# Kernel optimization log

Hardware: AMD Instinct MI355X
Metric: run time of the kernel (lower is better)

The kernel has to match this reference:

```python
import jax, jax.numpy as jnp
import numpy as np

IN_C, OUT_C, K, UP, C_DIM = 128, 64, 3, 2, 512
CLAMP = 256.0
ACT_GAIN = np.sqrt(2.0)  # lrelu def_gain


def _upfirdn_up2(x, f2):
    """upfirdn2d with up=2, padding=(3,2,3,2), gain=up^2 for a 4-tap filter.

    Padding values come from conv2d_resample: p = k//2 = 1, fw = 4, up = 2 =>
    px0 = p + (fw+up-1)//2 = 3, px1 = p + (fw-up)//2 = 2.
    """
    N, C, H, W = x.shape
    px0, px1 = 3, 2
    # zero-insert upsample (interior padding) fused with edge padding;
    # trailing zero of the up-sampled signal folded into the high pad.
    x = jax.lax.pad(x, jnp.asarray(0, x.dtype),
                    ((0, 0, 0), (0, 0, 0),
                     (px0, px1 + (UP - 1), UP - 1),
                     (px0, px1 + (UP - 1), UP - 1)))
    k = (f2 * (UP * UP)).astype(x.dtype)[None, None]   # [1,1,4,4], symmetric -> flip is a no-op
    k = jnp.tile(k, (C, 1, 1, 1))                       # depthwise FIR
    return jax.lax.conv_general_dilated(
        x, k, window_strides=(1, 1), padding='VALID',
        feature_group_count=C, dimension_numbers=('NCHW', 'OIHW', 'NCHW'))


def setup_inputs() -> dict:
    key = jax.random.key(0)
    ks = jax.random.split(key, 4)
    return {
        "x": jax.random.normal(ks[0], (8, IN_C, 128, 128), jnp.float32),
        "c": jax.random.normal(ks[1], (8, C_DIM), jnp.float32),
        "weight": jax.random.normal(ks[2], (OUT_C, IN_C, K, K), jnp.float32),
        "bias": jnp.zeros((OUT_C,), jnp.float32),
        "w_affine": jax.random.normal(ks[3], (IN_C, C_DIM), jnp.float32),
        "b_affine": jnp.zeros((IN_C,), jnp.float32),
    }


def reference(x, c, weight, bias, w_affine, b_affine):
    # setup_filter: normalize separable FIR taps
    f1 = jnp.array([1.0, 3.0, 3.0, 1.0], jnp.float32)
    f1 = f1 / jnp.sum(f1)
    f2 = jnp.outer(f1, f1)

    # hyper modulation: x *= 1 + tanh(affine(c))
    y = c @ (w_affine * (1.0 / np.sqrt(C_DIM))).T + b_affine   # FullyConnectedLayer, linear
    x = x * (1.0 + jnp.tanh(y))[:, :, None, None]

    # conv2d_resample(up=2, padding=k//2, flip_weight=False)
    w = weight * (1.0 / np.sqrt(IN_C * K * K))                  # weight_gain
    x = _upfirdn_up2(x, f2)                                      # [N,C,2H+2,2W+2]
    w = w[:, :, ::-1, ::-1]                                      # flip_weight=False => true convolution
    x = jax.lax.conv_general_dilated(
        x, w.astype(x.dtype), window_strides=(1, 1), padding='VALID',
        dimension_numbers=('NCHW', 'OIHW', 'NCHW'))              # [N,OUT_C,2H,2W]

    # bias_act: lrelu(x+b)*sqrt(2), clamp at +-256 (gain=1)
    x = jax.nn.leaky_relu(x + bias[None, :, None, None], 0.2) * ACT_GAIN
    return jnp.clip(x, -CLAMP, CLAMP)
```

## Files before the change

kernel.cpp:

```cpp
#include <hip/hip_runtime.h>
#include <math.h>

#define IN_C   128
#define OUT_C  64
#define CDIM   512
#define HW     128
#define PHW    130
#define OHW    256
#define NB     8

typedef __attribute__((ext_vector_type(8))) short short8;
typedef __attribute__((ext_vector_type(4))) float f32x4;

__device__ inline unsigned short f2bf(float f) {
    unsigned int u = __float_as_uint(f);
    unsigned int r = (u + 0x7fffu + ((u >> 16) & 1u)) >> 16;
    return (unsigned short)r;
}

__device__ inline float postact(float v) {
    v = v > 0.f ? v : 0.2f * v;
    v *= 1.4142135623730951f;
    return fminf(fmaxf(v, -256.f), 256.f);
}

__device__ __forceinline__ void gload16(const void* g, void* l) {
    __builtin_amdgcn_global_load_lds(
        (const __attribute__((address_space(1))) unsigned int*)g,
        (__attribute__((address_space(3))) unsigned int*)l, 16, 0, 0);
}

__global__ __launch_bounds__(256) void prep_kernel(
    const float* __restrict__ w, unsigned short* __restrict__ wb2,
    unsigned short* __restrict__ xg,
    const float* __restrict__ c, const float* __restrict__ wa,
    const float* __restrict__ ba, float* __restrict__ gain) {
    int blk = blockIdx.x;
    if (blk < 1152) {
        int idx  = blk * 256 + threadIdx.x;
        int e    = idx & 7;
        int lane = (idx >> 3) & 63;
        int pr   = (idx >> 9) & 31;
        int kt   = idx >> 14;
        int hh = pr >> 4, kcb = (pr >> 3) & 1, wM = (pr >> 2) & 1, fi = pr & 3;
        int m   = (wM * 8 + hh * 4 + fi) * 16 + (lane & 15);
        int ic  = (kt & 1) * 64 + kcb * 32 + (lane >> 4) * 8 + e;
        int tap = kt >> 1;
        int ky = tap / 3, kx = tap % 3;
        int oc = m >> 2, ph = m & 3;
        int py = ph >> 1, px = ph & 1;
        int sy = 2 * ky + (py == 0 ? 1 : 0);
        int sx = 2 * kx + (px == 0 ? 1 : 0);
        const float k1[4] = {0.25f, 0.75f, 0.75f, 0.25f};
        float sum = 0.f;
        #pragma unroll
        for (int by = 0; by < 3; ++by) {
            int ay = sy - by;
            if (ay < 0 || ay > 3) continue;
            #pragma unroll
            for (int bx = 0; bx < 3; ++bx) {
                int ax = sx - bx;
                if (ax < 0 || ax > 3) continue;
                sum += w[((oc * IN_C + ic) * 3 + (2 - by)) * 3 + (2 - bx)] * k1[ay] * k1[ax];
            }
        }
        wb2[idx] = f2bf(sum * 0.029462782549439483f);
    } else if (blk < 1410) {
        int id = (blk - 1152) * 256 + threadIdx.x;
        int cc = id & 15;
        int t  = id >> 4;
        int p  = t % 516;
        int n  = t / 516;
        int Y, X;
        if (p < 130)      { Y = 0;   X = p; }
        else if (p < 260) { Y = 129; X = p - 130; }
        else              { int q = p - 260; Y = 1 + (q >> 1); X = (q & 1) * 129; }
        uint4 z = make_uint4(0, 0, 0, 0);
        *reinterpret_cast<uint4*>(xg + (((size_t)(n * PHW) + Y) * PHW + X) * 128 + cc * 8) = z;
    } else {
        int wave = (blk - 1410) * 4 + (threadIdx.x >> 6);
        int lane = threadIdx.x & 63;
        int n  = wave >> 7;
        int ic = wave & 127;
        const float* cp = c + n * CDIM;
        const float* wp = wa + ic * CDIM;
        float s = 0.f;
        #pragma unroll
        for (int k = 0; k < CDIM / 64; ++k) s += cp[lane + 64 * k] * wp[lane + 64 * k];
        #pragma unroll
        for (int off = 32; off > 0; off >>= 1) s += __shfl_down(s, off);
        if (lane == 0) {
            float y = s * 0.04419417382415922f + ba[ic];
            gain[n * IN_C + ic] = 1.0f + tanhf(y);
        }
    }
}

__global__ __launch_bounds__(256) void xprep_kernel(const float* __restrict__ x,
                                                    const float* __restrict__ gain,
                                                    unsigned short* __restrict__ xg) {
    int n = blockIdx.x >> 7;
    int y = blockIdx.x & 127;
    __shared__ unsigned short lds[128][130];
    int tid = threadIdx.x;
    for (int i = tid; i < 128 * 128; i += 256) {
        int ic = i >> 7, pix = i & 127;
        float v = x[(((n * IN_C + ic) * HW) + y) * HW + pix] * gain[n * IN_C + ic];
        lds[pix][ic] = f2bf(v);
    }
    __syncthreads();
    unsigned int* dst = (unsigned int*)(xg + (((size_t)(n * PHW) + y + 1) * PHW + 1) * 128);
    for (int i = tid; i < 8192; i += 256) {
        int pix = i >> 6, d = i & 63;
        int j = d >> 2, ww = d & 3;
        int js = j ^ ((pix + 1) & 7);
        dst[pix * 64 + js * 4 + ww] = *reinterpret_cast<const unsigned int*>(&lds[pix][d * 2]);
    }
}

#define BARRIER() do { __builtin_amdgcn_sched_barrier(0); __builtin_amdgcn_s_barrier(); __builtin_amdgcn_sched_barrier(0); } while (0)
#define MM(ACC, AF, BF) ACC = __builtin_amdgcn_mfma_f32_16x16x32_bf16(AF, BF, ACC, 0, 0, 0)

__global__ __launch_bounds__(512, 2) void conv_mfma4(
    const unsigned short* __restrict__ xg,
    const unsigned short* __restrict__ wb2,
    const float* __restrict__ bias,
    float* __restrict__ out) {
    __shared__ __align__(16) char smem[148480];

    const int bid = blockIdx.x;
    const int wg  = ((bid & 7) << 6) + (bid >> 3);
    const int n     = wg >> 6;
    const int patch = wg & 63;
    const int Y0 = (patch >> 3) * 16;
    const int X0 = (patch & 7) * 16;
    const int tid  = threadIdx.x;
    const int lane = tid & 63;
    const int wid  = tid >> 6;
    const int wM = wid >> 2;
    const int wN = wid & 3;
    const int l16 = lane & 15;
    const int lhi = lane >> 4;
    const int pbase = wN * 4;

    const char* xgb = (const char*)xg + (size_t)n * PHW * PHW * 256;
    const char* wbb = (const char*)wb2;
    char* haloB = smem + 65536;

    #pragma unroll 1
    for (int i = 0; i < 11; ++i) {
        int cc = i * 512 + tid;
        if (cc < 5184) {
            int r = cc / 288;
            int t2 = cc - r * 288;
            gload16(xgb + ((size_t)(Y0 + r) * PHW + X0) * 256 + t2 * 16,
                    haloB + (i * 512 + wid * 64) * 16);
        }
    }

    auto stageA = [&](int k, int hh, int half) {
        gload16(wbb + k * 32768 + hh * 16384 + half * 8192 + tid * 16,
                smem + ((k & 1) << 15) + hh * 16384 + half * 8192 + wid * 1024);
    };

    f32x4 acc[8][4];
    #pragma unroll
    for (int f = 0; f < 8; ++f)
        #pragma unroll
        for (int b = 0; b < 4; ++b) acc[f][b] = (f32x4)0.f;

    stageA(0, 0, 0); stageA(0, 0, 1);
    stageA(0, 1, 0); stageA(0, 1, 1);
    stageA(1, 0, 0); stageA(1, 0, 1);
    asm volatile("s_waitcnt vmcnt(4)" ::: "memory");
    BARRIER();

    #pragma unroll 1
    for (int t = 0; t < 18; ++t) {
        const char* bA = smem + ((t & 1) << 15);
        const int tap = t >> 1;
        const int h   = t & 1;
        const int ky  = tap / 3;
        const int kx  = tap - ky * 3;
        const int C   = l16 + kx;
        const int bswz = (C & 7) << 4;

        auto ldB1 = [&](int b, int kc) -> short8 {
            int icoff = ((h << 7) + (kc << 6) + (lhi << 4)) ^ bswz;
            return *reinterpret_cast<const short8*>(
                haloB + ((pbase + b + ky) * 18 + C) * 256 + icoff);
        };

        short8 Af[8], Bf0[4], Bf1[4];

        #pragma unroll
        for (int f = 0; f < 4; ++f)
            #pragma unroll
            for (int kc = 0; kc < 2; ++kc)
                Af[f * 2 + kc] = *reinterpret_cast<const short8*>(
                    bA + ((kc * 8 + wM * 4 + f) << 10) + (lane << 4));
        #pragma unroll
        for (int b = 0; b < 2; ++b)
            #pragma unroll
            for (int kc = 0; kc < 2; ++kc) Bf0[b * 2 + kc] = ldB1(b, kc);
        if (t + 1 < 18) stageA(t + 1, 1, 0);
        BARRIER();
        __builtin_amdgcn_s_setprio(1);
        #pragma unroll
        for (int f = 0; f < 4; ++f)
            #pragma unroll
            for (int b = 0; b < 2; ++b) {
                MM(acc[f][b], Af[f * 2 + 0], Bf0[b * 2 + 0]);
                MM(acc[f][b], Af[f * 2 + 1], Bf0[b * 2 + 1]);
            }
        __builtin_amdgcn_s_setprio(0);

        #pragma unroll
        for (int b = 0; b < 2; ++b)
            #pragma unroll
            for (int kc = 0; kc < 2; ++kc) Bf1[b * 2 + kc] = ldB1(b + 2, kc);
        if (t + 1 < 18) stageA(t + 1, 1, 1);
        if (t < 17) { asm volatile("s_waitcnt vmcnt(4)" ::: "memory"); }
        else        { asm volatile("s_waitcnt vmcnt(0)" ::: "memory"); }
        BARRIER();
        __builtin_amdgcn_s_setprio(1);
        #pragma unroll
        for (int f = 0; f < 4; ++f)
            #pragma unroll
            for (int b = 0; b < 2; ++b) {
                MM(acc[f][b + 2], Af[f * 2 + 0], Bf1[b * 2 + 0]);
                MM(acc[f][b + 2], Af[f * 2 + 1], Bf1[b * 2 + 1]);
            }
        __builtin_amdgcn_s_setprio(0);

        #pragma unroll
        for (int f = 0; f < 4; ++f)
            #pragma unroll
            for (int kc = 0; kc < 2; ++kc)
                Af[f * 2 + kc] = *reinterpret_cast<const short8*>(
                    bA + ((16 + kc * 8 + wM * 4 + f) << 10) + (lane << 4));
        if (t + 2 < 18) stageA(t + 2, 0, 0);
        BARRIER();
        __builtin_amdgcn_s_setprio(1);
        #pragma unroll
        for (int f = 0; f < 4; ++f)
            #pragma unroll
            for (int b = 0; b < 2; ++b) {
                MM(acc[4 + f][b], Af[f * 2 + 0], Bf0[b * 2 + 0]);
                MM(acc[4 + f][b], Af[f * 2 + 1], Bf0[b * 2 + 1]);
            }
        __builtin_amdgcn_s_setprio(0);

        if (t + 2 < 18) stageA(t + 2, 0, 1);
        if (t < 16)       { asm volatile("s_waitcnt vmcnt(4)" ::: "memory"); }
        else if (t == 16) { asm volatile("s_waitcnt vmcnt(2)" ::: "memory"); }
        BARRIER();
        __builtin_amdgcn_s_setprio(1);
        #pragma unroll
        for (int f = 0; f < 4; ++f)
            #pragma unroll
            for (int b = 0; b < 2; ++b) {
                MM(acc[4 + f][b + 2], Af[f * 2 + 0], Bf1[b * 2 + 0]);
                MM(acc[4 + f][b + 2], Af[f * 2 + 1], Bf1[b * 2 + 1]);
            }
        __builtin_amdgcn_s_setprio(0);
    }

    #pragma unroll
    for (int f = 0; f < 8; ++f) {
        const int oc = wM * 32 + f * 4 + lhi;
        const float bi = bias[oc];
        #pragma unroll
        for (int b = 0; b < 4; ++b) {
            const int ypix = Y0 + pbase + b;
            const int xpix = X0 + l16;
            float* o0 = out + (((size_t)(n * OUT_C + oc) * OHW) + 2 * ypix) * OHW + 2 * xpix;
            float2 v0 = make_float2(postact(acc[f][b][0] + bi), postact(acc[f][b][1] + bi));
            float2 v1 = make_float2(postact(acc[f][b][2] + bi), postact(acc[f][b][3] + bi));
            *reinterpret_cast<float2*>(o0) = v0;
            *reinterpret_cast<float2*>(o0 + OHW) = v1;
        }
    }
}

__global__ void gain_kernel(const float* __restrict__ c,
                            const float* __restrict__ w_affine,
                            const float* __restrict__ b_affine,
                            float* __restrict__ gain) {
    int wave = (blockIdx.x * blockDim.x + threadIdx.x) >> 6;
    int lane = threadIdx.x & 63;
    if (wave >= NB * IN_C) return;
    int n  = wave >> 7;
    int ic = wave & 127;
    const float* cp = c + n * CDIM;
    const float* wp = w_affine + ic * CDIM;
    float s = 0.f;
    #pragma unroll
    for (int k = 0; k < CDIM / 64; ++k) s += cp[lane + 64 * k] * wp[lane + 64 * k];
    #pragma unroll
    for (int off = 32; off > 0; off >>= 1) s += __shfl_down(s, off);
    if (lane == 0) {
        float y = s * 0.04419417382415922f + b_affine[ic];
        gain[n * IN_C + ic] = 1.0f + tanhf(y);
    }
}

__global__ void wprep_kernel(const float* __restrict__ w, float* __restrict__ wp) {
    int idx = blockIdx.x * blockDim.x + threadIdx.x;
    if (idx >= IN_C * 9 * 4 * OUT_C) return;
    int oc = idx & 63;
    int t  = idx >> 6;
    int ph = t & 3;  t >>= 2;
    int kx = t % 3;  t /= 3;
    int ky = t % 3;  t /= 3;
    int ic = t;
    int py = ph >> 1, px = ph & 1;
    int sy = 2 * ky + (py == 0 ? 1 : 0);
    int sx = 2 * kx + (px == 0 ? 1 : 0);
    const float k1[4] = {0.25f, 0.75f, 0.75f, 0.25f};
    float sum = 0.f;
    #pragma unroll
    for (int by = 0; by < 3; ++by) {
        int ay = sy - by;
        if (ay < 0 || ay > 3) continue;
        #pragma unroll
        for (int bx = 0; bx < 3; ++bx) {
            int ax = sx - bx;
            if (ax < 0 || ax > 3) continue;
            sum += w[((oc * IN_C + ic) * 3 + (2 - by)) * 3 + (2 - bx)] * k1[ay] * k1[ax];
        }
    }
    wp[idx] = sum * 0.029462782549439483f;
}

__global__ __launch_bounds__(256) void conv_main(
    const float* __restrict__ x, const float* __restrict__ gain,
    const float* __restrict__ wp, const float* __restrict__ bias,
    float* __restrict__ out) {
    const int n    = blockIdx.z >> 3;
    const int occ  = (blockIdx.z & 7) * 8;
    const int tx0  = blockIdx.x * 16;
    const int ty0  = blockIdx.y * 16;
    const int tid  = threadIdx.x;
    const int lx   = tid & 15;
    const int ly   = tid >> 4;
    __shared__ float xsf[8][18][18];
    float acc[4][8];
    #pragma unroll
    for (int p = 0; p < 4; ++p)
        #pragma unroll
        for (int o = 0; o < 8; ++o) acc[p][o] = 0.f;
    for (int ic0 = 0; ic0 < IN_C; ic0 += 8) {
        __syncthreads();
        for (int i = tid; i < 8 * 324; i += 256) {
            int icb = i / 324;
            int rem = i - icb * 324;
            int yy  = rem / 18;
            int xx  = rem - yy * 18;
            int gy  = ty0 + yy - 1;
            int gx  = tx0 + xx - 1;
            int ic  = ic0 + icb;
            float v = 0.f;
            if (gy >= 0 && gy < HW && gx >= 0 && gx < HW)
                v = x[((n * IN_C + ic) * HW + gy) * HW + gx] * gain[n * IN_C + ic];
            xsf[icb][yy][xx] = v;
        }
        __syncthreads();
        for (int icb = 0; icb < 8; ++icb) {
            const int ic = ic0 + icb;
            const float* wpp = wp + ic * (9 * 4 * OUT_C) + occ;
            #pragma unroll
            for (int ky = 0; ky < 3; ++ky)
                #pragma unroll
                for (int kx = 0; kx < 3; ++kx) {
                    float tv = xsf[icb][ly + ky][lx + kx];
                    const float* w9 = wpp + (ky * 3 + kx) * (4 * OUT_C);
                    #pragma unroll
                    for (int p = 0; p < 4; ++p)
                        #pragma unroll
                        for (int o = 0; o < 8; ++o)
                            acc[p][o] = fmaf(tv, w9[p * OUT_C + o], acc[p][o]);
                }
        }
    }
    const int ybase = 2 * (ty0 + ly);
    const int xbase = 2 * (tx0 + lx);
    #pragma unroll
    for (int o = 0; o < 8; ++o) {
        float b = bias[occ + o];
        #pragma unroll
        for (int py = 0; py < 2; ++py) {
            float2 v;
            v.x = postact(acc[py * 2 + 0][o] + b);
            v.y = postact(acc[py * 2 + 1][o] + b);
            *reinterpret_cast<float2*>(
                &out[((size_t)(n * OUT_C + occ + o) * OHW + (ybase + py)) * OHW + xbase]) = v;
        }
    }
}

extern "C" void kernel_launch(void* const* d_in, const int* in_sizes, int n_in,
                              void* d_out, int out_size, void* d_ws, size_t ws_size,
                              hipStream_t stream) {
    const float* x        = (const float*)d_in[0];
    const float* c        = (const float*)d_in[1];
    const float* weight   = (const float*)d_in[2];
    const float* bias     = (const float*)d_in[3];
    const float* w_affine = (const float*)d_in[4];
    const float* b_affine = (const float*)d_in[5];
    float* out = (float*)d_out;

    float* gain = (float*)d_ws;

    const size_t NEED = 1048576 + (size_t)NB * PHW * PHW * IN_C * 2;
    if (ws_size >= NEED) {
        unsigned short* wb2 = (unsigned short*)((char*)d_ws + 8192);
        unsigned short* xg  = (unsigned short*)((char*)d_ws + 1048576);
        prep_kernel<<<dim3(1666), dim3(256), 0, stream>>>(weight, wb2, xg, c, w_affine, b_affine, gain);
        xprep_kernel<<<dim3(NB * HW), dim3(256), 0, stream>>>(x, gain, xg);
        conv_mfma4<<<dim3(512), dim3(512), 0, stream>>>(xg, wb2, bias, out);
    } else {
        float* wp = (float*)((char*)d_ws + 8192);
        gain_kernel<<<dim3((NB * IN_C * 64) / 256), dim3(256), 0, stream>>>(c, w_affine, b_affine, gain);
        wprep_kernel<<<dim3((IN_C * 9 * 4 * OUT_C + 255) / 256), dim3(256), 0, stream>>>(weight, wp);
        conv_main<<<dim3(HW / 16, HW / 16, NB * 8), dim3(256), 0, stream>>>(x, gain, wp, bias, out);
    }
}
```

Baseline: 105.1 us.

## Load weight fragments directly from global memory instead of LDS double buffering

The conv kernel no longer stages weight (A) tiles into shared memory through a double-buffered pipeline with barriers and manual waitcnt. Each wave now reads its A fragments straight from global/L2 per tap and runs all 64 MFMAs per step in one block, with no per-phase barriers. This removes LDS traffic, barriers and priority switching, and cuts LDS use to the halo only, which could allow more blocks per CU. In exchange, global load latency is exposed on every iteration with no software prefetch, and the weight reads are repeated across waves.

```diff
diff --git a/kernel.cpp b/kernel.cpp
--- a/kernel.cpp
+++ b/kernel.cpp
@@ -118,15 +118,14 @@
     }
 }
 
-#define BARRIER() do { __builtin_amdgcn_sched_barrier(0); __builtin_amdgcn_s_barrier(); __builtin_amdgcn_sched_barrier(0); } while (0)
 #define MM(ACC, AF, BF) ACC = __builtin_amdgcn_mfma_f32_16x16x32_bf16(AF, BF, ACC, 0, 0, 0)
 
-__global__ __launch_bounds__(512, 2) void conv_mfma4(
+__global__ __launch_bounds__(512, 2) void conv_mfma5(
     const unsigned short* __restrict__ xg,
     const unsigned short* __restrict__ wb2,
     const float* __restrict__ bias,
     float* __restrict__ out) {
-    __shared__ __align__(16) char smem[148480];
+    __shared__ __align__(16) char haloB[82944];
 
     const int bid = blockIdx.x;
     const int wg  = ((bid & 7) << 6) + (bid >> 3);
@@ -144,8 +143,6 @@
     const int pbase = wN * 4;
 
     const char* xgb = (const char*)xg + (size_t)n * PHW * PHW * 256;
-    const char* wbb = (const char*)wb2;
-    char* haloB = smem + 65536;
 
     #pragma unroll 1
     for (int i = 0; i < 11; ++i) {
@@ -158,10 +155,7 @@
         }
     }
 
-    auto stageA = [&](int k, int hh, int half) {
-        gload16(wbb + k * 32768 + hh * 16384 + half * 8192 + tid * 16,
-                smem + ((k & 1) << 15) + hh * 16384 + half * 8192 + wid * 1024);
-    };
+    const char* abase = (const char*)wb2 + (wM << 12) + (lane << 4);
 
     f32x4 acc[8][4];
     #pragma unroll
@@ -169,101 +163,41 @@
         #pragma unroll
         for (int b = 0; b < 4; ++b) acc[f][b] = (f32x4)0.f;
 
-    stageA(0, 0, 0); stageA(0, 0, 1);
-    stageA(0, 1, 0); stageA(0, 1, 1);
-    stageA(1, 0, 0); stageA(1, 0, 1);
-    asm volatile("s_waitcnt vmcnt(4)" ::: "memory");
-    BARRIER();
+    __syncthreads();
 
     #pragma unroll 1
     for (int t = 0; t < 18; ++t) {
-        const char* bA = smem + ((t & 1) << 15);
         const int tap = t >> 1;
         const int h   = t & 1;
         const int ky  = tap / 3;
         const int kx  = tap - ky * 3;
         const int C   = l16 + kx;
         const int bswz = (C & 7) << 4;
-
-        auto ldB1 = [&](int b, int kc) -> short8 {
-            int icoff = ((h << 7) + (kc << 6) + (lhi << 4)) ^ bswz;
-            return *reinterpret_cast<const short8*>(
-                haloB + ((pbase + b + ky) * 18 + C) * 256 + icoff);
-        };
-
-        short8 Af[8], Bf0[4], Bf1[4];
-
-        #pragma unroll
-        for (int f = 0; f < 4; ++f)
-            #pragma unroll
-            for (int kc = 0; kc < 2; ++kc)
-                Af[f * 2 + kc] = *reinterpret_cast<const short8*>(
-                    bA + ((kc * 8 + wM * 4 + f) << 10) + (lane << 4));
-        #pragma unroll
-        for (int b = 0; b < 2; ++b)
-            #pragma unroll
-            for (int kc = 0; kc < 2; ++kc) Bf0[b * 2 + kc] = ldB1(b, kc);
-        if (t + 1 < 18) stageA(t + 1, 1, 0);
-        BARRIER();
-        __builtin_amdgcn_s_setprio(1);
-        #pragma unroll
-        for (int f = 0; f < 4; ++f)
-            #pragma unroll
-            for (int b = 0; b < 2; ++b) {
-                MM(acc[f][b], Af[f * 2 + 0], Bf0[b * 2 + 0]);
-                MM(acc[f][b], Af[f * 2 + 1], Bf0[b * 2 + 1]);
+        const char* ak = abase + t * 32768;
+
+        short8 Af[8][2];
+        short8 Bf[4][2];
+        #pragma unroll
+        for (int kc = 0; kc < 2; ++kc)
+            #pragma unroll
+            for (int f = 0; f < 8; ++f)
+                Af[f][kc] = *reinterpret_cast<const short8*>(
+                    ak + ((((f >> 2) << 4) + (kc << 3) + (f & 3)) << 10));
+        #pragma unroll
+        for (int kc = 0; kc < 2; ++kc)
+            #pragma unroll
+            for (int b = 0; b < 4; ++b) {
+                int icoff = ((h << 7) + (kc << 6) + (lhi << 4)) ^ bswz;
+                Bf[b][kc] = *reinterpret_cast<const short8*>(
+                    haloB + ((pbase + b + ky) * 18 + C) * 256 + icoff);
             }
-        __builtin_amdgcn_s_setprio(0);
-
-        #pragma unroll
-        for (int b = 0; b < 2; ++b)
-            #pragma unroll
-            for (int kc = 0; kc < 2; ++kc) Bf1[b * 2 + kc] = ldB1(b + 2, kc);
-        if (t + 1 < 18) stageA(t + 1, 1, 1);
-        if (t < 17) { asm volatile("s_waitcnt vmcnt(4)" ::: "memory"); }
-        else        { asm volatile("s_waitcnt vmcnt(0)" ::: "memory"); }
-        BARRIER();
-        __builtin_amdgcn_s_setprio(1);
-        #pragma unroll
-        for (int f = 0; f < 4; ++f)
-            #pragma unroll
-            for (int b = 0; b < 2; ++b) {
-                MM(acc[f][b + 2], Af[f * 2 + 0], Bf1[b * 2 + 0]);
-                MM(acc[f][b + 2], Af[f * 2 + 1], Bf1[b * 2 + 1]);
-            }
-        __builtin_amdgcn_s_setprio(0);
-
-        #pragma unroll
-        for (int f = 0; f < 4; ++f)
-            #pragma unroll
-            for (int kc = 0; kc < 2; ++kc)
-                Af[f * 2 + kc] = *reinterpret_cast<const short8*>(
-                    bA + ((16 + kc * 8 + wM * 4 + f) << 10) + (lane << 4));
-        if (t + 2 < 18) stageA(t + 2, 0, 0);
-        BARRIER();
-        __builtin_amdgcn_s_setprio(1);
-        #pragma unroll
-        for (int f = 0; f < 4; ++f)
-            #pragma unroll
-            for (int b = 0; b < 2; ++b) {
-                MM(acc[4 + f][b], Af[f * 2 + 0], Bf0[b * 2 + 0]);
-                MM(acc[4 + f][b], Af[f * 2 + 1], Bf0[b * 2 + 1]);
-            }
-        __builtin_amdgcn_s_setprio(0);
-
-        if (t + 2 < 18) stageA(t + 2, 0, 1);
-        if (t < 16)       { asm volatile("s_waitcnt vmcnt(4)" ::: "memory"); }
-        else if (t == 16) { asm volatile("s_waitcnt vmcnt(2)" ::: "memory"); }
-        BARRIER();
-        __builtin_amdgcn_s_setprio(1);
-        #pragma unroll
-        for (int f = 0; f < 4; ++f)
-            #pragma unroll
-            for (int b = 0; b < 2; ++b) {
-                MM(acc[4 + f][b + 2], Af[f * 2 + 0], Bf1[b * 2 + 0]);
-                MM(acc[4 + f][b + 2], Af[f * 2 + 1], Bf1[b * 2 + 1]);
-            }
-        __builtin_amdgcn_s_setprio(0);
+        #pragma unroll
+        for (int kc = 0; kc < 2; ++kc)
+            #pragma unroll
+            for (int f = 0; f < 8; ++f)
+                #pragma unroll
+                for (int b = 0; b < 4; ++b)
+                    MM(acc[f][b], Af[f][kc], Bf[b][kc]);
     }
 
     #pragma unroll
@@ -418,7 +352,7 @@
         unsigned short* xg  = (unsigned short*)((char*)d_ws + 1048576);
         prep_kernel<<<dim3(1666), dim3(256), 0, stream>>>(weight, wb2, xg, c, w_affine, b_affine, gain);
         xprep_kernel<<<dim3(NB * HW), dim3(256), 0, stream>>>(x, gain, xg);
-        conv_mfma4<<<dim3(512), dim3(512), 0, stream>>>(xg, wb2, bias, out);
+        conv_mfma5<<<dim3(512), dim3(512), 0, stream>>>(xg, wb2, bias, out);
     } else {
         float* wp = (float*)((char*)d_ws + 8192);
         gain_kernel<<<dim3((NB * IN_C * 64) / 256), dim3(256), 0, stream>>>(c, w_affine, b_affine, gain);
```

Measured after the change: 127.4 us. 21.3% more time.
